# Kernel optimization log

Hardware: AMD Instinct MI355X
Metric: run time of the kernel (lower is better)

The kernel has to match this reference:

```python
import jax, jax.numpy as jnp
import numpy as np

B, T, J, D = 16, 2048, 128, 1024


def setup_inputs() -> dict:
    key = jax.random.key(0)
    k1, k2, k3, k4 = jax.random.split(key, 4)
    H = jax.random.normal(k1, (B, T, D), dtype=jnp.float32)
    U = jax.random.normal(k2, (B, J, D), dtype=jnp.float32)
    # nn.Linear(3*D, 1): weight [1, 3*D], bias [1]
    w_hu_w = jax.random.normal(k3, (1, 3 * D), dtype=jnp.float32) / np.sqrt(3 * D)
    w_hu_b = jax.random.normal(k4, (1,), dtype=jnp.float32) * 0.01
    return {"H": H, "U": U, "w_hu_w": w_hu_w, "w_hu_b": w_hu_b}


def reference(H, U, w_hu_w, w_hu_b):
    # Original math: scores1[b,t,j] = w . [H_bt ; U_bj ; H_bt * U_bj] + bias.
    # Decompose w into (w1, w2, w3) so the O(B*T*J*3D) intermediate is never built.
    d = H.shape[-1]
    w = w_hu_w[0]
    w1, w2, w3 = w[:d], w[d:2 * d], w[2 * d:]
    scores1 = (
        (H @ w1)[:, :, None]                      # [B,T,1]
        + (U @ w2)[:, None, :]                    # [B,1,J]
        + jnp.einsum("btd,bjd->btj", H * w3, U)  # elementwise term
        + w_hu_b[0]
    )  # [B,T,J]

    att1 = jax.nn.softmax(scores1, axis=2)            # softmax over query dim
    att2 = jax.nn.softmax(scores1.max(axis=2), axis=1)[:, None, :]  # [B,1,T]

    agg1 = jnp.einsum("btj,bjd->btd", att1, U)        # [B,T,D]
    agg2 = jnp.einsum("bot,btd->bod", att2, H)        # [B,1,D]
    agg2 = jnp.broadcast_to(agg2, H.shape)            # expand to [B,T,D]

    G = jnp.concatenate([H, agg1, H * agg1, H * agg2], axis=2)  # [B,T,4D]
    return att1, att2, G
```

## Files before the change

kernel.cpp:

```cpp
#include <hip/hip_runtime.h>

#define B_ 16
#define T_ 2048
#define J_ 128
#define D_ 1024

#define WS_UWB  0
#define WS_AGG2 2048
#define WSB_VH  73728UL
#define WSB_VL  (WSB_VH  + 4194304UL)
#define WSB_UTH (WSB_VL  + 4194304UL)
#define WSB_UTL (WSB_UTH + 4194304UL)

#define OFF_ATT1 0
#define OFF_ATT2 4194304UL
#define OFF_G    4227072UL

typedef float4 f4;
typedef unsigned short u16;
typedef unsigned int u32;
typedef __attribute__((ext_vector_type(8))) short short8;
typedef __attribute__((ext_vector_type(4))) float fx4;

#define MFMA(A, B, C) __builtin_amdgcn_mfma_f32_16x16x32_bf16(A, B, C, 0, 0, 0)

__device__ __forceinline__ u16 f2bf(float f) {
    u32 u = __float_as_uint(f);
    u = (u + 0x7fffu + ((u >> 16) & 1u)) >> 16;
    return (u16)u;
}
__device__ __forceinline__ float bf2f(u16 h) { return __uint_as_float((u32)h << 16); }

__device__ __forceinline__ void split8(f4 a, f4 b, short8& h8, short8& l8) {
    float x[8] = {a.x, a.y, a.z, a.w, b.x, b.y, b.z, b.w};
#pragma unroll
    for (int i = 0; i < 8; ++i) {
        u16 h = f2bf(x[i]);
        u16 l = f2bf(x[i] - bf2f(h));
        h8[i] = (short)h;
        l8[i] = (short)l;
    }
}

__global__ __launch_bounds__(256) void k_prep(const float* __restrict__ U,
                                              const float* __restrict__ w,
                                              u16* __restrict__ Vh, u16* __restrict__ Vl,
                                              u16* __restrict__ Uth, u16* __restrict__ Utl) {
    const int b = blockIdx.y;
    const int j0 = blockIdx.x * 16;
    const int tid = threadIdx.x;
#pragma unroll
    for (int q = 0; q < 4; ++q) {
        int d = q * 256 + tid;
        float w3 = w[2 * D_ + d];
        u32 ph[8], pl[8];
#pragma unroll
        for (int jj = 0; jj < 16; ++jj) {
            size_t gi = ((size_t)(b * J_ + j0 + jj)) * D_ + d;
            float uval = U[gi];
            u16 uh = f2bf(uval);
            u16 ul = f2bf(uval - bf2f(uh));
            if (jj & 1) { ph[jj >> 1] |= (u32)uh << 16; pl[jj >> 1] |= (u32)ul << 16; }
            else        { ph[jj >> 1] = uh;             pl[jj >> 1] = ul; }
            float v = uval * w3;
            u16 vh = f2bf(v);
            Vh[gi] = vh;
            Vl[gi] = f2bf(v - bf2f(vh));
        }
        u16* tp = Uth + ((size_t)(b * D_ + d)) * J_ + j0;
        *(uint4*)tp       = make_uint4(ph[0], ph[1], ph[2], ph[3]);
        *(uint4*)(tp + 8) = make_uint4(ph[4], ph[5], ph[6], ph[7]);
        u16* lp = Utl + ((size_t)(b * D_ + d)) * J_ + j0;
        *(uint4*)lp       = make_uint4(pl[0], pl[1], pl[2], pl[3]);
        *(uint4*)(lp + 8) = make_uint4(pl[4], pl[5], pl[6], pl[7]);
    }
}

__global__ __launch_bounds__(256) void k_uwb(const float* __restrict__ U,
                                             const float* __restrict__ w,
                                             const float* __restrict__ bias,
                                             float* __restrict__ ws) {
    int bj = blockIdx.x;
    const float* Urow = U + (size_t)bj * D_;
    const float* w2 = w + D_;
    float s = 0.f;
    for (int i = threadIdx.x; i < D_; i += 256) s = fmaf(Urow[i], w2[i], s);
#pragma unroll
    for (int off = 32; off > 0; off >>= 1) s += __shfl_down(s, off, 64);
    __shared__ float red[4];
    if ((threadIdx.x & 63) == 0) red[threadIdx.x >> 6] = s;
    __syncthreads();
    if (threadIdx.x == 0)
        ws[WS_UWB + bj] = red[0] + red[1] + red[2] + red[3] + bias[0];
}

struct __align__(16) SMemM {
    union {
        struct { u16 Hh[64][72]; u16 Hl[64][72]; u16 Vh[128][72]; u16 Vl[128][72]; } g1;
        struct { float P[64][132]; u16 Uh[64][136]; u16 Ul[64][136]; } g2;
    } u;
    float uwbs[J_];
    float hw[64];
};

__global__ __launch_bounds__(256) void k_main(const float* __restrict__ H,
                                              const float* __restrict__ w,
                                              const float* __restrict__ wsf,
                                              const u16* __restrict__ Vhg,
                                              const u16* __restrict__ Vlg,
                                              const u16* __restrict__ Uthg,
                                              const u16* __restrict__ Utlg,
                                              float* __restrict__ out) {
    __shared__ SMemM sm;
    const int tid = threadIdx.x;
    const int lane = tid & 63;
    const int wv = tid >> 6;
    const int lr = lane & 15;
    const int lg = lane >> 4;
    const int b = blockIdx.y;
    const int t0 = blockIdx.x * 64;
    const float* Hb = H + ((size_t)b * T_ + t0) * D_;

    if (tid < J_) sm.uwbs[tid] = wsf[WS_UWB + b * J_ + tid];

    fx4 acc[8] = {};
    float hwacc0 = 0.f, hwacc1 = 0.f;

    const int srow = tid >> 3;
    const int sk8  = (tid & 7) * 8;

#pragma unroll 1
    for (int d0 = 0; d0 < D_; d0 += 64) {
        __syncthreads();
        f4 wa = *(const f4*)(w + d0 + sk8);
        f4 wb = *(const f4*)(w + d0 + sk8 + 4);
        {
            const float* hp = Hb + (size_t)srow * D_ + d0 + sk8;
            f4 a = *(const f4*)hp; f4 c = *(const f4*)(hp + 4);
            hwacc0 = fmaf(a.x, wa.x, hwacc0); hwacc0 = fmaf(a.y, wa.y, hwacc0);
            hwacc0 = fmaf(a.z, wa.z, hwacc0); hwacc0 = fmaf(a.w, wa.w, hwacc0);
            hwacc0 = fmaf(c.x, wb.x, hwacc0); hwacc0 = fmaf(c.y, wb.y, hwacc0);
            hwacc0 = fmaf(c.z, wb.z, hwacc0); hwacc0 = fmaf(c.w, wb.w, hwacc0);
            short8 h8, l8; split8(a, c, h8, l8);
            *(short8*)&sm.u.g1.Hh[srow][sk8] = h8;
            *(short8*)&sm.u.g1.Hl[srow][sk8] = l8;
        }
        {
            const float* hp = Hb + (size_t)(srow + 32) * D_ + d0 + sk8;
            f4 a = *(const f4*)hp; f4 c = *(const f4*)(hp + 4);
            hwacc1 = fmaf(a.x, wa.x, hwacc1); hwacc1 = fmaf(a.y, wa.y, hwacc1);
            hwacc1 = fmaf(a.z, wa.z, hwacc1); hwacc1 = fmaf(a.w, wa.w, hwacc1);
            hwacc1 = fmaf(c.x, wb.x, hwacc1); hwacc1 = fmaf(c.y, wb.y, hwacc1);
            hwacc1 = fmaf(c.z, wb.z, hwacc1); hwacc1 = fmaf(c.w, wb.w, hwacc1);
            short8 h8, l8; split8(a, c, h8, l8);
            *(short8*)&sm.u.g1.Hh[srow + 32][sk8] = h8;
            *(short8*)&sm.u.g1.Hl[srow + 32][sk8] = l8;
        }
#pragma unroll
        for (int q = 0; q < 4; ++q) {
            int slot = tid + q * 256;
            int row = slot >> 3;
            int k8 = (slot & 7) * 8;
            size_t gi = ((size_t)(b * J_ + row)) * D_ + d0 + k8;
            *(uint4*)&sm.u.g1.Vh[row][k8] = *(const uint4*)(Vhg + gi);
            *(uint4*)&sm.u.g1.Vl[row][k8] = *(const uint4*)(Vlg + gi);
        }
        __syncthreads();
#pragma unroll
        for (int ks = 0; ks < 2; ++ks) {
            int kk = ks * 32 + lg * 8;
            short8 ah = *(const short8*)&sm.u.g1.Hh[wv * 16 + lr][kk];
            short8 al = *(const short8*)&sm.u.g1.Hl[wv * 16 + lr][kk];
#pragma unroll
            for (int n = 0; n < 8; ++n) {
                short8 bh = *(const short8*)&sm.u.g1.Vh[n * 16 + lr][kk];
                short8 bl = *(const short8*)&sm.u.g1.Vl[n * 16 + lr][kk];
                acc[n] = MFMA(ah, bh, acc[n]);
                acc[n] = MFMA(ah, bl, acc[n]);
                acc[n] = MFMA(al, bh, acc[n]);
            }
        }
    }

#pragma unroll
    for (int off = 1; off < 8; off <<= 1) {
        hwacc0 += __shfl_xor(hwacc0, off, 64);
        hwacc1 += __shfl_xor(hwacc1, off, 64);
    }
    if ((tid & 7) == 0) { sm.hw[srow] = hwacc0; sm.hw[srow + 32] = hwacc1; }
    __syncthreads();

    float* att1o = out + OFF_ATT1 + ((size_t)(b * T_ + t0 + wv * 16)) * J_;
    float* m_out = out + OFF_ATT2 + (size_t)b * T_ + t0 + wv * 16;
#pragma unroll
    for (int r = 0; r < 4; ++r) {
        float mx = -1e30f;
#pragma unroll
        for (int n = 0; n < 8; ++n) {
            float s = acc[n][r] + sm.uwbs[n * 16 + lr];
            acc[n][r] = s;
            mx = fmaxf(mx, s);
        }
#pragma unroll
        for (int off = 1; off < 16; off <<= 1) mx = fmaxf(mx, __shfl_xor(mx, off, 64));
        float sum = 0.f;
#pragma unroll
        for (int n = 0; n < 8; ++n) { float e = __expf(acc[n][r] - mx); acc[n][r] = e; sum += e; }
#pragma unroll
        for (int off = 1; off < 16; off <<= 1) sum += __shfl_xor(sum, off, 64);
        float inv = 1.f / sum;
        int row = lg * 4 + r;
#pragma unroll
        for (int n = 0; n < 8; ++n) {
            float p = acc[n][r] * inv;
            att1o[(size_t)row * J_ + n * 16 + lr] = p;
            sm.u.g2.P[wv * 16 + row][n * 16 + lr] = p;
        }
        if (lr == 0) m_out[row] = mx + sm.hw[wv * 16 + row];
    }
    __syncthreads();

    short8 pha[4], pla[4];
#pragma unroll
    for (int ks = 0; ks < 4; ++ks) {
        const float* pp = &sm.u.g2.P[wv * 16 + lr][ks * 32 + lg * 8];
        f4 p0 = *(const f4*)pp;
        f4 p1 = *(const f4*)(pp + 4);
        split8(p0, p1, pha[ks], pla[ks]);
    }

    float* Gb = out + OFF_G + ((size_t)(b * T_ + t0)) * 4096;
#pragma unroll 1
    for (int d0 = 0; d0 < D_; d0 += 64) {
        __syncthreads();
#pragma unroll
        for (int q = 0; q < 4; ++q) {
            int slot = tid + q * 256;
            int row = slot >> 4;
            int j8 = (slot & 15) * 8;
            size_t gi = ((size_t)(b * D_ + d0 + row)) * J_ + j8;
            *(uint4*)&sm.u.g2.Uh[row][j8] = *(const uint4*)(Uthg + gi);
            *(uint4*)&sm.u.g2.Ul[row][j8] = *(const uint4*)(Utlg + gi);
        }
        __syncthreads();
        fx4 a2[4] = {};
#pragma unroll
        for (int ks = 0; ks < 4; ++ks) {
            int kk = ks * 32 + lg * 8;
#pragma unroll
            for (int n = 0; n < 4; ++n) {
                short8 bh = *(const short8*)&sm.u.g2.Uh[n * 16 + lr][kk];
                short8 bl = *(const short8*)&sm.u.g2.Ul[n * 16 + lr][kk];
                a2[n] = MFMA(pha[ks], bh, a2[n]);
                a2[n] = MFMA(pha[ks], bl, a2[n]);
                a2[n] = MFMA(pla[ks], bh, a2[n]);
            }
        }
#pragma unroll
        for (int n = 0; n < 4; ++n) {
#pragma unroll
            for (int r = 0; r < 4; ++r) {
                int row = wv * 16 + lg * 4 + r;
                int d = d0 + n * 16 + lr;
                float h = Hb[(size_t)row * D_ + d];
                float a = a2[n][r];
                float* g = Gb + (size_t)row * 4096 + d;
                g[0]    = h;
                g[1024] = a;
                g[2048] = h * a;
            }
        }
    }
}

__global__ __launch_bounds__(256) void k_att2(float* __restrict__ out) {
    int b = blockIdx.x, tid = threadIdx.x;
    float* mptr = out + OFF_ATT2 + (size_t)b * T_;
    float mv[8];
    float mx = -1e30f;
#pragma unroll
    for (int k = 0; k < 8; ++k) { mv[k] = mptr[tid + k * 256]; mx = fmaxf(mx, mv[k]); }
#pragma unroll
    for (int off = 1; off < 64; off <<= 1) mx = fmaxf(mx, __shfl_xor(mx, off, 64));
    __shared__ float redm[4], reds[4];
    if ((tid & 63) == 0) redm[tid >> 6] = mx;
    __syncthreads();
    float M = fmaxf(fmaxf(redm[0], redm[1]), fmaxf(redm[2], redm[3]));
    float s = 0.f;
#pragma unroll
    for (int k = 0; k < 8; ++k) { mv[k] = __expf(mv[k] - M); s += mv[k]; }
#pragma unroll
    for (int off = 1; off < 64; off <<= 1) s += __shfl_xor(s, off, 64);
    if ((tid & 63) == 0) reds[tid >> 6] = s;
    __syncthreads();
    float inv = 1.f / (reds[0] + reds[1] + reds[2] + reds[3]);
#pragma unroll
    for (int k = 0; k < 8; ++k) mptr[tid + k * 256] = mv[k] * inv;
}

__global__ __launch_bounds__(256) void k_agg2(const float* __restrict__ H,
                                              const float* __restrict__ att2,
                                              float* __restrict__ ws) {
    int b = blockIdx.y;
    int d0 = blockIdx.x * 64;
    int c = threadIdx.x & 63;
    int tq = threadIdx.x >> 6;
    const float* Hb = H + (size_t)b * T_ * D_;
    const float* a2 = att2 + (size_t)b * T_;
    float acc = 0.f;
#pragma unroll 8
    for (int t = tq; t < T_; t += 4)
        acc = fmaf(a2[t], Hb[(size_t)t * D_ + d0 + c], acc);
    __shared__ float red[4][64];
    red[tq][c] = acc;
    __syncthreads();
    if (tq == 0)
        ws[WS_AGG2 + b * D_ + d0 + c] = red[0][c] + red[1][c] + red[2][c] + red[3][c];
}

__global__ __launch_bounds__(256) void k_chunk3(const float* __restrict__ H,
                                                const float* __restrict__ ws,
                                                float* __restrict__ out) {
    size_t id = (size_t)blockIdx.x * 256 + threadIdx.x;
    int d4 = (int)(id & 255);
    int t  = (int)((id >> 8) & 2047);
    int b  = (int)(id >> 19);
    f4 h = *(const f4*)(H + id * 4);
    f4 a = *(const f4*)(ws + WS_AGG2 + b * D_ + d4 * 4);
    f4 r = make_float4(h.x * a.x, h.y * a.y, h.z * a.z, h.w * a.w);
    *(f4*)(out + OFF_G + ((size_t)(b * T_ + t)) * 4096 + 3072 + d4 * 4) = r;
}

extern "C" void kernel_launch(void* const* d_in, const int* in_sizes, int n_in,
                              void* d_out, int out_size, void* d_ws, size_t ws_size,
                              hipStream_t stream) {
    const float* H    = (const float*)d_in[0];
    const float* U    = (const float*)d_in[1];
    const float* w    = (const float*)d_in[2];
    const float* bias = (const float*)d_in[3];
    float* out = (float*)d_out;
    float* ws  = (float*)d_ws;
    u16* wsVh  = (u16*)((char*)d_ws + WSB_VH);
    u16* wsVl  = (u16*)((char*)d_ws + WSB_VL);
    u16* wsUth = (u16*)((char*)d_ws + WSB_UTH);
    u16* wsUtl = (u16*)((char*)d_ws + WSB_UTL);

    k_prep  <<<dim3(J_ / 16, B_), dim3(256), 0, stream>>>(U, w, wsVh, wsVl, wsUth, wsUtl);
    k_uwb   <<<dim3(B_ * J_),     dim3(256), 0, stream>>>(U, w, bias, ws);
    k_main  <<<dim3(T_ / 64, B_), dim3(256), 0, stream>>>(H, w, ws, wsVh, wsVl, wsUth, wsUtl, out);
    k_att2  <<<dim3(B_),          dim3(256), 0, stream>>>(out);
    k_agg2  <<<dim3(D_ / 64, B_), dim3(256), 0, stream>>>(H, out + OFF_ATT2, ws);
    k_chunk3<<<dim3((B_ * T_ * (D_ / 4)) / 256), dim3(256), 0, stream>>>(H, ws, out);
}
```

Measured before the change: 835.6 us.

## Prefetch global tiles into registers, swizzle LDS, fuse U·w2 into prep, remap blocks per XCD

The main kernel now loads the next 64-wide slice of H and V (and later U-transpose) into registers while MFMAs run on the current slice, overlapping global latency with compute. LDS tiles drop their padding and use an XOR swizzle to avoid bank conflicts, and the second GEMM swaps operand order so G writes become float4-vectorised rows. The U·w2 reduction is folded into the prep kernel, removing one launch. Blocks are remapped so each XCD handles whole batches, k_main gets a 2-blocks-per-CU launch bound, and agg2 uses 512 threads. The register prefetch raises register pressure and could limit occupancy.

```diff
diff --git a/kernel.cpp b/kernel.cpp
--- a/kernel.cpp
+++ b/kernel.cpp
@@ -44,20 +44,27 @@
 
 __global__ __launch_bounds__(256) void k_prep(const float* __restrict__ U,
                                               const float* __restrict__ w,
+                                              const float* __restrict__ bias,
                                               u16* __restrict__ Vh, u16* __restrict__ Vl,
-                                              u16* __restrict__ Uth, u16* __restrict__ Utl) {
+                                              u16* __restrict__ Uth, u16* __restrict__ Utl,
+                                              float* __restrict__ ws) {
     const int b = blockIdx.y;
     const int j0 = blockIdx.x * 16;
     const int tid = threadIdx.x;
+    float uacc[16];
+#pragma unroll
+    for (int jj = 0; jj < 16; ++jj) uacc[jj] = 0.f;
 #pragma unroll
     for (int q = 0; q < 4; ++q) {
         int d = q * 256 + tid;
         float w3 = w[2 * D_ + d];
+        float w2 = w[D_ + d];
         u32 ph[8], pl[8];
 #pragma unroll
         for (int jj = 0; jj < 16; ++jj) {
             size_t gi = ((size_t)(b * J_ + j0 + jj)) * D_ + d;
             float uval = U[gi];
+            uacc[jj] = fmaf(uval, w2, uacc[jj]);
             u16 uh = f2bf(uval);
             u16 ul = f2bf(uval - bf2f(uh));
             if (jj & 1) { ph[jj >> 1] |= (u32)uh << 16; pl[jj >> 1] |= (u32)ul << 16; }
@@ -74,51 +81,49 @@
         *(uint4*)lp       = make_uint4(pl[0], pl[1], pl[2], pl[3]);
         *(uint4*)(lp + 8) = make_uint4(pl[4], pl[5], pl[6], pl[7]);
     }
-}
-
-__global__ __launch_bounds__(256) void k_uwb(const float* __restrict__ U,
-                                             const float* __restrict__ w,
-                                             const float* __restrict__ bias,
-                                             float* __restrict__ ws) {
-    int bj = blockIdx.x;
-    const float* Urow = U + (size_t)bj * D_;
-    const float* w2 = w + D_;
-    float s = 0.f;
-    for (int i = threadIdx.x; i < D_; i += 256) s = fmaf(Urow[i], w2[i], s);
-#pragma unroll
-    for (int off = 32; off > 0; off >>= 1) s += __shfl_down(s, off, 64);
-    __shared__ float red[4];
-    if ((threadIdx.x & 63) == 0) red[threadIdx.x >> 6] = s;
-    __syncthreads();
-    if (threadIdx.x == 0)
-        ws[WS_UWB + bj] = red[0] + red[1] + red[2] + red[3] + bias[0];
+    __shared__ float ured[16][4];
+    const int lane = tid & 63, wvq = tid >> 6;
+#pragma unroll
+    for (int jj = 0; jj < 16; ++jj) {
+        float s = uacc[jj];
+#pragma unroll
+        for (int off = 32; off > 0; off >>= 1) s += __shfl_down(s, off, 64);
+        if (lane == 0) ured[jj][wvq] = s;
+    }
+    __syncthreads();
+    if (tid < 16)
+        ws[WS_UWB + b * J_ + j0 + tid] =
+            ured[tid][0] + ured[tid][1] + ured[tid][2] + ured[tid][3] + bias[0];
 }
 
 struct __align__(16) SMemM {
     union {
-        struct { u16 Hh[64][72]; u16 Hl[64][72]; u16 Vh[128][72]; u16 Vl[128][72]; } g1;
-        struct { float P[64][132]; u16 Uh[64][136]; u16 Ul[64][136]; } g2;
+        struct { u16 Hh[64][64]; u16 Hl[64][64]; u16 Vh[128][64]; u16 Vl[128][64]; } g1;
+        struct { float P[64][132]; u16 Uh[64][128]; u16 Ul[64][128]; } g2;
     } u;
     float uwbs[J_];
     float hw[64];
 };
 
-__global__ __launch_bounds__(256) void k_main(const float* __restrict__ H,
-                                              const float* __restrict__ w,
-                                              const float* __restrict__ wsf,
-                                              const u16* __restrict__ Vhg,
-                                              const u16* __restrict__ Vlg,
-                                              const u16* __restrict__ Uthg,
-                                              const u16* __restrict__ Utlg,
-                                              float* __restrict__ out) {
+__global__ __launch_bounds__(256, 2) void k_main(const float* __restrict__ H,
+                                                 const float* __restrict__ w,
+                                                 const float* __restrict__ wsf,
+                                                 const u16* __restrict__ Vhg,
+                                                 const u16* __restrict__ Vlg,
+                                                 const u16* __restrict__ Uthg,
+                                                 const u16* __restrict__ Utlg,
+                                                 float* __restrict__ out) {
     __shared__ SMemM sm;
     const int tid = threadIdx.x;
     const int lane = tid & 63;
     const int wv = tid >> 6;
     const int lr = lane & 15;
     const int lg = lane >> 4;
-    const int b = blockIdx.y;
-    const int t0 = blockIdx.x * 64;
+    const int bid = blockIdx.x;
+    const int xcd = bid & 7;
+    const int kk_ = bid >> 3;
+    const int b = xcd + ((kk_ >> 5) << 3);
+    const int t0 = (kk_ & 31) * 64;
     const float* Hb = H + ((size_t)b * T_ + t0) * D_;
 
     if (tid < J_) sm.uwbs[tid] = wsf[WS_UWB + b * J_ + tid];
@@ -127,54 +132,73 @@
     float hwacc0 = 0.f, hwacc1 = 0.f;
 
     const int srow = tid >> 3;
-    const int sk8  = (tid & 7) * 8;
-
+    const int soc  = tid & 7;
+    const int sk8  = soc * 8;
+
+    f4 hA0, hC0, hA1, hC1;
+    uint4 pv[8];
+    auto LOADG1 = [&](int d0) {
+        const float* hp0 = Hb + (size_t)srow * D_ + d0 + sk8;
+        hA0 = *(const f4*)hp0; hC0 = *(const f4*)(hp0 + 4);
+        const float* hp1 = Hb + (size_t)(srow + 32) * D_ + d0 + sk8;
+        hA1 = *(const f4*)hp1; hC1 = *(const f4*)(hp1 + 4);
+#pragma unroll
+        for (int q = 0; q < 4; ++q) {
+            int slot = tid + q * 256;
+            int row = slot >> 3;
+            int k8 = (slot & 7) * 8;
+            size_t gi = ((size_t)(b * J_ + row)) * D_ + d0 + k8;
+            pv[q]     = *(const uint4*)(Vhg + gi);
+            pv[q + 4] = *(const uint4*)(Vlg + gi);
+        }
+    };
+
+    LOADG1(0);
 #pragma unroll 1
     for (int d0 = 0; d0 < D_; d0 += 64) {
         __syncthreads();
         f4 wa = *(const f4*)(w + d0 + sk8);
         f4 wb = *(const f4*)(w + d0 + sk8 + 4);
+        hwacc0 = fmaf(hA0.x, wa.x, hwacc0); hwacc0 = fmaf(hA0.y, wa.y, hwacc0);
+        hwacc0 = fmaf(hA0.z, wa.z, hwacc0); hwacc0 = fmaf(hA0.w, wa.w, hwacc0);
+        hwacc0 = fmaf(hC0.x, wb.x, hwacc0); hwacc0 = fmaf(hC0.y, wb.y, hwacc0);
+        hwacc0 = fmaf(hC0.z, wb.z, hwacc0); hwacc0 = fmaf(hC0.w, wb.w, hwacc0);
+        hwacc1 = fmaf(hA1.x, wa.x, hwacc1); hwacc1 = fmaf(hA1.y, wa.y, hwacc1);
+        hwacc1 = fmaf(hA1.z, wa.z, hwacc1); hwacc1 = fmaf(hA1.w, wa.w, hwacc1);
+        hwacc1 = fmaf(hC1.x, wb.x, hwacc1); hwacc1 = fmaf(hC1.y, wb.y, hwacc1);
+        hwacc1 = fmaf(hC1.z, wb.z, hwacc1); hwacc1 = fmaf(hC1.w, wb.w, hwacc1);
         {
-            const float* hp = Hb + (size_t)srow * D_ + d0 + sk8;
-            f4 a = *(const f4*)hp; f4 c = *(const f4*)(hp + 4);
-            hwacc0 = fmaf(a.x, wa.x, hwacc0); hwacc0 = fmaf(a.y, wa.y, hwacc0);
-            hwacc0 = fmaf(a.z, wa.z, hwacc0); hwacc0 = fmaf(a.w, wa.w, hwacc0);
-            hwacc0 = fmaf(c.x, wb.x, hwacc0); hwacc0 = fmaf(c.y, wb.y, hwacc0);
-            hwacc0 = fmaf(c.z, wb.z, hwacc0); hwacc0 = fmaf(c.w, wb.w, hwacc0);
-            short8 h8, l8; split8(a, c, h8, l8);
-            *(short8*)&sm.u.g1.Hh[srow][sk8] = h8;
-            *(short8*)&sm.u.g1.Hl[srow][sk8] = l8;
+            short8 h8, l8; split8(hA0, hC0, h8, l8);
+            int so = (soc ^ (srow & 7)) * 8;
+            *(short8*)&sm.u.g1.Hh[srow][so] = h8;
+            *(short8*)&sm.u.g1.Hl[srow][so] = l8;
         }
         {
-            const float* hp = Hb + (size_t)(srow + 32) * D_ + d0 + sk8;
-            f4 a = *(const f4*)hp; f4 c = *(const f4*)(hp + 4);
-            hwacc1 = fmaf(a.x, wa.x, hwacc1); hwacc1 = fmaf(a.y, wa.y, hwacc1);
-            hwacc1 = fmaf(a.z, wa.z, hwacc1); hwacc1 = fmaf(a.w, wa.w, hwacc1);
-            hwacc1 = fmaf(c.x, wb.x, hwacc1); hwacc1 = fmaf(c.y, wb.y, hwacc1);
-            hwacc1 = fmaf(c.z, wb.z, hwacc1); hwacc1 = fmaf(c.w, wb.w, hwacc1);
-            short8 h8, l8; split8(a, c, h8, l8);
-            *(short8*)&sm.u.g1.Hh[srow + 32][sk8] = h8;
-            *(short8*)&sm.u.g1.Hl[srow + 32][sk8] = l8;
+            short8 h8, l8; split8(hA1, hC1, h8, l8);
+            int so = (soc ^ (srow & 7)) * 8;
+            *(short8*)&sm.u.g1.Hh[srow + 32][so] = h8;
+            *(short8*)&sm.u.g1.Hl[srow + 32][so] = l8;
         }
 #pragma unroll
         for (int q = 0; q < 4; ++q) {
             int slot = tid + q * 256;
             int row = slot >> 3;
-            int k8 = (slot & 7) * 8;
-            size_t gi = ((size_t)(b * J_ + row)) * D_ + d0 + k8;
-            *(uint4*)&sm.u.g1.Vh[row][k8] = *(const uint4*)(Vhg + gi);
-            *(uint4*)&sm.u.g1.Vl[row][k8] = *(const uint4*)(Vlg + gi);
+            int oc = slot & 7;
+            int so = (oc ^ (row & 7)) * 8;
+            *(uint4*)&sm.u.g1.Vh[row][so] = pv[q];
+            *(uint4*)&sm.u.g1.Vl[row][so] = pv[q + 4];
         }
         __syncthreads();
+        if (d0 + 64 < D_) LOADG1(d0 + 64);
 #pragma unroll
         for (int ks = 0; ks < 2; ++ks) {
-            int kk = ks * 32 + lg * 8;
-            short8 ah = *(const short8*)&sm.u.g1.Hh[wv * 16 + lr][kk];
-            short8 al = *(const short8*)&sm.u.g1.Hl[wv * 16 + lr][kk];
+            int oct = (ks * 4 + lg) ^ (lr & 7);
+            short8 ah = *(const short8*)&sm.u.g1.Hh[wv * 16 + lr][oct * 8];
+            short8 al = *(const short8*)&sm.u.g1.Hl[wv * 16 + lr][oct * 8];
 #pragma unroll
             for (int n = 0; n < 8; ++n) {
-                short8 bh = *(const short8*)&sm.u.g1.Vh[n * 16 + lr][kk];
-                short8 bl = *(const short8*)&sm.u.g1.Vl[n * 16 + lr][kk];
+                short8 bh = *(const short8*)&sm.u.g1.Vh[n * 16 + lr][oct * 8];
+                short8 bl = *(const short8*)&sm.u.g1.Vl[n * 16 + lr][oct * 8];
                 acc[n] = MFMA(ah, bh, acc[n]);
                 acc[n] = MFMA(ah, bl, acc[n]);
                 acc[n] = MFMA(al, bh, acc[n]);
@@ -189,6 +213,20 @@
     }
     if ((tid & 7) == 0) { sm.hw[srow] = hwacc0; sm.hw[srow + 32] = hwacc1; }
     __syncthreads();
+
+    uint4 uv[8];
+    auto LOADG2 = [&](int d0) {
+#pragma unroll
+        for (int q = 0; q < 4; ++q) {
+            int slot = tid + q * 256;
+            int row = slot >> 4;
+            int j8 = (slot & 15) * 8;
+            size_t gi = ((size_t)(b * D_ + d0 + row)) * J_ + j8;
+            uv[q]     = *(const uint4*)(Uthg + gi);
+            uv[q + 4] = *(const uint4*)(Utlg + gi);
+        }
+    };
+    LOADG2(0);
 
     float* att1o = out + OFF_ATT1 + ((size_t)(b * T_ + t0 + wv * 16)) * J_;
     float* m_out = out + OFF_ATT2 + (size_t)b * T_ + t0 + wv * 16;
@@ -237,37 +275,40 @@
         for (int q = 0; q < 4; ++q) {
             int slot = tid + q * 256;
             int row = slot >> 4;
-            int j8 = (slot & 15) * 8;
-            size_t gi = ((size_t)(b * D_ + d0 + row)) * J_ + j8;
-            *(uint4*)&sm.u.g2.Uh[row][j8] = *(const uint4*)(Uthg + gi);
-            *(uint4*)&sm.u.g2.Ul[row][j8] = *(const uint4*)(Utlg + gi);
+            int oc = slot & 15;
+            int so = ((oc & 8) | ((oc ^ row) & 7)) * 8;
+            *(uint4*)&sm.u.g2.Uh[row][so] = uv[q];
+            *(uint4*)&sm.u.g2.Ul[row][so] = uv[q + 4];
         }
         __syncthreads();
+        if (d0 + 64 < D_) LOADG2(d0 + 64);
         fx4 a2[4] = {};
 #pragma unroll
         for (int ks = 0; ks < 4; ++ks) {
-            int kk = ks * 32 + lg * 8;
-#pragma unroll
-            for (int n = 0; n < 4; ++n) {
-                short8 bh = *(const short8*)&sm.u.g2.Uh[n * 16 + lr][kk];
-                short8 bl = *(const short8*)&sm.u.g2.Ul[n * 16 + lr][kk];
-                a2[n] = MFMA(pha[ks], bh, a2[n]);
-                a2[n] = MFMA(pha[ks], bl, a2[n]);
-                a2[n] = MFMA(pla[ks], bh, a2[n]);
+            int o = ks * 4 + lg;
+#pragma unroll
+            for (int mt = 0; mt < 4; ++mt) {
+                int rr = mt * 16 + lr;
+                int so = ((o & 8) | ((o ^ rr) & 7)) * 8;
+                short8 uh = *(const short8*)&sm.u.g2.Uh[rr][so];
+                short8 ul = *(const short8*)&sm.u.g2.Ul[rr][so];
+                a2[mt] = MFMA(uh, pha[ks], a2[mt]);
+                a2[mt] = MFMA(uh, pla[ks], a2[mt]);
+                a2[mt] = MFMA(ul, pha[ks], a2[mt]);
             }
         }
-#pragma unroll
-        for (int n = 0; n < 4; ++n) {
-#pragma unroll
-            for (int r = 0; r < 4; ++r) {
-                int row = wv * 16 + lg * 4 + r;
-                int d = d0 + n * 16 + lr;
-                float h = Hb[(size_t)row * D_ + d];
-                float a = a2[n][r];
-                float* g = Gb + (size_t)row * 4096 + d;
-                g[0]    = h;
-                g[1024] = a;
-                g[2048] = h * a;
+        {
+            int trow = wv * 16 + lr;
+            const float* hp = Hb + (size_t)trow * D_ + d0 + lg * 4;
+            float* g = Gb + (size_t)trow * 4096 + d0 + lg * 4;
+#pragma unroll
+            for (int mt = 0; mt < 4; ++mt) {
+                fx4 h4 = *(const fx4*)(hp + mt * 16);
+                fx4 a4 = a2[mt];
+                fx4 m4 = h4 * a4;
+                *(fx4*)(g + mt * 16)        = h4;
+                *(fx4*)(g + mt * 16 + 1024) = a4;
+                *(fx4*)(g + mt * 16 + 2048) = m4;
             }
         }
     }
@@ -298,7 +339,7 @@
     for (int k = 0; k < 8; ++k) mptr[tid + k * 256] = mv[k] * inv;
 }
 
-__global__ __launch_bounds__(256) void k_agg2(const float* __restrict__ H,
+__global__ __launch_bounds__(512) void k_agg2(const float* __restrict__ H,
                                               const float* __restrict__ att2,
                                               float* __restrict__ ws) {
     int b = blockIdx.y;
@@ -309,13 +350,17 @@
     const float* a2 = att2 + (size_t)b * T_;
     float acc = 0.f;
 #pragma unroll 8
-    for (int t = tq; t < T_; t += 4)
+    for (int t = tq; t < T_; t += 8)
         acc = fmaf(a2[t], Hb[(size_t)t * D_ + d0 + c], acc);
-    __shared__ float red[4][64];
+    __shared__ float red[8][64];
     red[tq][c] = acc;
     __syncthreads();
-    if (tq == 0)
-        ws[WS_AGG2 + b * D_ + d0 + c] = red[0][c] + red[1][c] + red[2][c] + red[3][c];
+    if (tq == 0) {
+        float s = 0.f;
+#pragma unroll
+        for (int k = 0; k < 8; ++k) s += red[k][c];
+        ws[WS_AGG2 + b * D_ + d0 + c] = s;
+    }
 }
 
 __global__ __launch_bounds__(256) void k_chunk3(const float* __restrict__ H,
@@ -345,10 +390,9 @@
     u16* wsUth = (u16*)((char*)d_ws + WSB_UTH);
     u16* wsUtl = (u16*)((char*)d_ws + WSB_UTL);
 
-    k_prep  <<<dim3(J_ / 16, B_), dim3(256), 0, stream>>>(U, w, wsVh, wsVl, wsUth, wsUtl);
-    k_uwb   <<<dim3(B_ * J_),     dim3(256), 0, stream>>>(U, w, bias, ws);
-    k_main  <<<dim3(T_ / 64, B_), dim3(256), 0, stream>>>(H, w, ws, wsVh, wsVl, wsUth, wsUtl, out);
+    k_prep  <<<dim3(J_ / 16, B_), dim3(256), 0, stream>>>(U, w, bias, wsVh, wsVl, wsUth, wsUtl, ws);
+    k_main  <<<dim3(512),         dim3(256), 0, stream>>>(H, w, ws, wsVh, wsVl, wsUth, wsUtl, out);
     k_att2  <<<dim3(B_),          dim3(256), 0, stream>>>(out);
-    k_agg2  <<<dim3(D_ / 64, B_), dim3(256), 0, stream>>>(H, out + OFF_ATT2, ws);
+    k_agg2  <<<dim3(D_ / 64, B_), dim3(512), 0, stream>>>(H, out + OFF_ATT2, ws);
     k_chunk3<<<dim3((B_ * T_ * (D_ / 4)) / 256), dim3(256), 0, stream>>>(H, ws, out);
 }
```

New measurement: 934.2 us. 1.12x slower.
